# Kernel tuning notes

Measured on AMD Instinct MI355X. Metric: run time of the kernel, lower is better.

Reference implementation:

```python
import jax, jax.numpy as jnp
import numpy as np

EPS = 1e-08
CJS_WEIGHT = 0.5  # init kwarg `weight`
B, C = 4096, 8192


def setup_inputs() -> dict:
    key = jax.random.key(0)
    k1, k2 = jax.random.split(key)
    pred_logit = jax.random.normal(k1, (B, C), dtype=jnp.float32)
    gt_raw = jax.random.uniform(k2, (B, C), dtype=jnp.float32) + EPS
    gt = gt_raw / jnp.sum(gt_raw, axis=1, keepdims=True)  # row-stochastic target distribution
    return {"pred_logit": pred_logit, "gt": gt}


def reference(pred_logit, gt):
    xlogy = jax.scipy.special.xlogy
    n, c = pred_logit.shape

    # CrossEntropyLoss with soft (probability) targets, mean over batch
    logp = jax.nn.log_softmax(pred_logit, axis=1)
    ce = -jnp.mean(jnp.sum(gt * logp, axis=1))

    # CJS loss: sum_{i=1..C} 0.5*(KL(D_{:i} || m_{:i}) + KL(P_{:i} || m_{:i})) / B
    # Column j contributes to every prefix i > j, i.e. with weight (C - j):
    # one fused weighted-sum pass instead of the O(C^2) prefix loop.
    p = jnp.exp(logp)                      # softmax(pred_logit)
    m = 0.5 * (gt + p + EPS)
    logm = jnp.log(m)
    contrib = (xlogy(gt, gt) - gt * logm) + (xlogy(p, p) - p * logm)  # [B, C]
    w = (c - jnp.arange(c)).astype(pred_logit.dtype)                   # prefix multiplicity
    cjs = 0.5 * jnp.sum(contrib * w) / n   # 'batchmean' divides by B

    return ce + CJS_WEIGHT * cjs
```

## Files before the change

### kernel.cpp

```cpp
#include <hip/hip_runtime.h>

#define EPSF 1e-8f
#define NROWS 4096
#define NCOLS 8192
#define TPB 256
#define F4_PER_LANE (NCOLS / 4 / 64)

__global__ __launch_bounds__(TPB) void cecjs_main(const float* __restrict__ pred,
                                                  const float* __restrict__ gt,
                                                  double2* __restrict__ partial) {
    const int lane = threadIdx.x & 63;
    const int row  = blockIdx.x * (TPB / 64) + (threadIdx.x >> 6);

    const float4* pr = (const float4*)(pred + (size_t)row * NCOLS);
    const float4* gr = (const float4*)(gt   + (size_t)row * NCOLS);

    float s = 0.f;
    #pragma unroll 4
    for (int i = 0; i < F4_PER_LANE; ++i) {
        float4 v = pr[lane + i * 64];
        s += (__expf(v.x) + __expf(v.y)) + (__expf(v.z) + __expf(v.w));
    }
    #pragma unroll
    for (int off = 1; off < 64; off <<= 1) s += __shfl_xor(s, off, 64);
    const float logsum = __logf(s);

    float ce = 0.f, cj = 0.f;
    #pragma unroll 4
    for (int i = 0; i < F4_PER_LANE; ++i) {
        float4 v  = pr[lane + i * 64];
        float4 g4 = gr[lane + i * 64];
        const int c0 = (lane + i * 64) * 4;
        #pragma unroll
        for (int k = 0; k < 4; ++k) {
            float x  = (&v.x)[k];
            float g  = (&g4.x)[k];
            float lp = x - logsum;
            float p  = __expf(lp);
            ce = fmaf(g, lp, ce);
            float m    = 0.5f * (g + p + EPSF);
            float logm = __logf(m);
            float contrib = g * (__logf(g) - logm) + p * (lp - logm);
            cj = fmaf(contrib, (float)(NCOLS - (c0 + k)), cj);
        }
    }
    #pragma unroll
    for (int off = 1; off < 64; off <<= 1) {
        ce += __shfl_xor(ce, off, 64);
        cj += __shfl_xor(cj, off, 64);
    }
    if (lane == 0) partial[row] = make_double2((double)ce, (double)cj);
}

__global__ __launch_bounds__(1024) void cecjs_final(const double2* __restrict__ partial,
                                                    float* __restrict__ out) {
    __shared__ double sce[16], scj[16];
    const int tid  = threadIdx.x;
    const int lane = tid & 63;
    const int wid  = tid >> 6;
    double ce = 0.0, cj = 0.0;
    #pragma unroll
    for (int i = tid; i < NROWS; i += 1024) {
        double2 d = partial[i];
        ce += d.x; cj += d.y;
    }
    #pragma unroll
    for (int off = 1; off < 64; off <<= 1) {
        ce += __shfl_xor(ce, off, 64);
        cj += __shfl_xor(cj, off, 64);
    }
    if (lane == 0) { sce[wid] = ce; scj[wid] = cj; }
    __syncthreads();
    if (tid == 0) {
        double a = 0.0, b = 0.0;
        #pragma unroll
        for (int i = 0; i < 16; ++i) { a += sce[i]; b += scj[i]; }
        out[0] = (float)((-a + 0.25 * b) / (double)NROWS);
    }
}

extern "C" void kernel_launch(void* const* d_in, const int* in_sizes, int n_in,
                              void* d_out, int out_size, void* d_ws, size_t ws_size,
                              hipStream_t stream) {
    const float* pred = (const float*)d_in[0];
    const float* gt   = (const float*)d_in[1];
    double2* partial  = (double2*)d_ws;
    cecjs_main<<<NROWS / (TPB / 64), TPB, 0, stream>>>(pred, gt, partial);
    cecjs_final<<<1, 1024, 0, stream>>>(partial, (float*)d_out);
}
```

Before: 281.5 us.

## Map one row per block and keep pred values and exps in registers

Each row is now handled by a 512-thread block instead of a single wavefront, and each thread holds its 16 pred values in registers. The second global read of pred goes away and the exponentials are reused, so p becomes exp times a reciprocal of the row sum instead of a second exp. Cross-wave reductions now go through shared memory with two block barriers. Register pressure rises, and the barriers add some synchronisation cost per row.

```diff
diff --git a/kernel.cpp b/kernel.cpp
--- a/kernel.cpp
+++ b/kernel.cpp
@@ -3,45 +3,61 @@
 #define EPSF 1e-8f
 #define NROWS 4096
 #define NCOLS 8192
-#define TPB 256
-#define F4_PER_LANE (NCOLS / 4 / 64)
+#define TPB 512
 
 __global__ __launch_bounds__(TPB) void cecjs_main(const float* __restrict__ pred,
                                                   const float* __restrict__ gt,
                                                   double2* __restrict__ partial) {
-    const int lane = threadIdx.x & 63;
-    const int row  = blockIdx.x * (TPB / 64) + (threadIdx.x >> 6);
+    __shared__ float  sA[8];
+    __shared__ double sce[8], scj[8];
+
+    const int row  = blockIdx.x;
+    const int tid  = threadIdx.x;
+    const int lane = tid & 63;
+    const int wid  = tid >> 6;
 
     const float4* pr = (const float4*)(pred + (size_t)row * NCOLS);
     const float4* gr = (const float4*)(gt   + (size_t)row * NCOLS);
 
+    float4 v[4], e[4];
     float s = 0.f;
-    #pragma unroll 4
-    for (int i = 0; i < F4_PER_LANE; ++i) {
-        float4 v = pr[lane + i * 64];
-        s += (__expf(v.x) + __expf(v.y)) + (__expf(v.z) + __expf(v.w));
+    #pragma unroll
+    for (int i = 0; i < 4; ++i) v[i] = pr[tid + i * TPB];
+    #pragma unroll
+    for (int i = 0; i < 4; ++i) {
+        e[i].x = __expf(v[i].x);
+        e[i].y = __expf(v[i].y);
+        e[i].z = __expf(v[i].z);
+        e[i].w = __expf(v[i].w);
+        s += (e[i].x + e[i].y) + (e[i].z + e[i].w);
     }
     #pragma unroll
     for (int off = 1; off < 64; off <<= 1) s += __shfl_xor(s, off, 64);
-    const float logsum = __logf(s);
+    if (lane == 0) sA[wid] = s;
+    __syncthreads();
+    float tot = 0.f;
+    #pragma unroll
+    for (int i = 0; i < 8; ++i) tot += sA[i];
+    const float logsum = __logf(tot);
+    const float invsum = 1.0f / tot;
 
     float ce = 0.f, cj = 0.f;
-    #pragma unroll 4
-    for (int i = 0; i < F4_PER_LANE; ++i) {
-        float4 v  = pr[lane + i * 64];
-        float4 g4 = gr[lane + i * 64];
-        const int c0 = (lane + i * 64) * 4;
+    #pragma unroll
+    for (int i = 0; i < 4; ++i) {
+        float4 g4 = gr[tid + i * TPB];
+        const float w0 = (float)(NCOLS - (tid + i * TPB) * 4);
         #pragma unroll
         for (int k = 0; k < 4; ++k) {
-            float x  = (&v.x)[k];
+            float x  = (&v[i].x)[k];
+            float ev = (&e[i].x)[k];
             float g  = (&g4.x)[k];
             float lp = x - logsum;
-            float p  = __expf(lp);
+            float p  = ev * invsum;
             ce = fmaf(g, lp, ce);
             float m    = 0.5f * (g + p + EPSF);
             float logm = __logf(m);
             float contrib = g * (__logf(g) - logm) + p * (lp - logm);
-            cj = fmaf(contrib, (float)(NCOLS - (c0 + k)), cj);
+            cj = fmaf(contrib, w0 - (float)k, cj);
         }
     }
     #pragma unroll
@@ -49,7 +65,14 @@
         ce += __shfl_xor(ce, off, 64);
         cj += __shfl_xor(cj, off, 64);
     }
-    if (lane == 0) partial[row] = make_double2((double)ce, (double)cj);
+    if (lane == 0) { sce[wid] = (double)ce; scj[wid] = (double)cj; }
+    __syncthreads();
+    if (tid == 0) {
+        double a = 0.0, b = 0.0;
+        #pragma unroll
+        for (int i = 0; i < 8; ++i) { a += sce[i]; b += scj[i]; }
+        partial[row] = make_double2(a, b);
+    }
 }
 
 __global__ __launch_bounds__(1024) void cecjs_final(const double2* __restrict__ partial,
@@ -85,6 +108,6 @@
     const float* pred = (const float*)d_in[0];
     const float* gt   = (const float*)d_in[1];
     double2* partial  = (double2*)d_ws;
-    cecjs_main<<<NROWS / (TPB / 64), TPB, 0, stream>>>(pred, gt, partial);
+    cecjs_main<<<NROWS, TPB, 0, stream>>>(pred, gt, partial);
     cecjs_final<<<1, 1024, 0, stream>>>(partial, (float*)d_out);
 }
```

New measurement: 277.5 us. About the same (-1.4%).

## Split row logsumexp into separate kernel and grid-stride the main elementwise pass

Applied to the files above, without the earlier changes.

Moves the per-row sum of exponentials into its own kernel, with one block per row, that writes log2 of the sum to workspace. The main kernel then walks the flattened arrays with a grid-stride loop over 2048 blocks, computing in base 2 with the native exp2/log2 intrinsics. It scales by ln2 once in the final reduction. This removes the one-wave-per-row serialization and mixes rows across blocks, at the cost of an extra launch and reading pred twice from global memory rather than from cache.

```diff
diff --git a/kernel.cpp b/kernel.cpp
--- a/kernel.cpp
+++ b/kernel.cpp
@@ -1,66 +1,98 @@
 #include <hip/hip_runtime.h>
 
-#define EPSF 1e-8f
-#define NROWS 4096
-#define NCOLS 8192
-#define TPB 256
-#define F4_PER_LANE (NCOLS / 4 / 64)
+#define EPSF   1e-8f
+#define NROWS  4096
+#define NCOLS  8192
+#define F4ROW  (NCOLS / 4)
+#define K2_BLOCKS 2048
+#define K2_TPB    256
+#define NTHREADS  (K2_BLOCKS * K2_TPB)
+#define ITERS     ((NROWS * F4ROW) / NTHREADS)
+#define LOG2E  1.44269504088896340736f
+#define LN2    0.693147180559945309417f
 
-__global__ __launch_bounds__(TPB) void cecjs_main(const float* __restrict__ pred,
-                                                  const float* __restrict__ gt,
-                                                  double2* __restrict__ partial) {
-    const int lane = threadIdx.x & 63;
-    const int row  = blockIdx.x * (TPB / 64) + (threadIdx.x >> 6);
+#if __has_builtin(__builtin_amdgcn_exp2f)
+#define EXP2F(x) __builtin_amdgcn_exp2f(x)
+#else
+#define EXP2F(x) exp2f(x)
+#endif
+#if __has_builtin(__builtin_amdgcn_logf)
+#define LOG2F(x) __builtin_amdgcn_logf(x)
+#else
+#define LOG2F(x) log2f(x)
+#endif
 
+__global__ __launch_bounds__(256) void k_rowsum(const float* __restrict__ pred,
+                                                float* __restrict__ ls2) {
+    __shared__ float sA[4];
+    const int row = blockIdx.x, tid = threadIdx.x, lane = tid & 63, wid = tid >> 6;
     const float4* pr = (const float4*)(pred + (size_t)row * NCOLS);
-    const float4* gr = (const float4*)(gt   + (size_t)row * NCOLS);
-
     float s = 0.f;
-    #pragma unroll 4
-    for (int i = 0; i < F4_PER_LANE; ++i) {
-        float4 v = pr[lane + i * 64];
-        s += (__expf(v.x) + __expf(v.y)) + (__expf(v.z) + __expf(v.w));
+    #pragma unroll
+    for (int i = 0; i < 8; ++i) {
+        float4 v = pr[tid + i * 256];
+        s += (EXP2F(v.x * LOG2E) + EXP2F(v.y * LOG2E))
+           + (EXP2F(v.z * LOG2E) + EXP2F(v.w * LOG2E));
     }
     #pragma unroll
     for (int off = 1; off < 64; off <<= 1) s += __shfl_xor(s, off, 64);
-    const float logsum = __logf(s);
+    if (lane == 0) sA[wid] = s;
+    __syncthreads();
+    if (tid == 0) ls2[row] = LOG2F(sA[0] + sA[1] + sA[2] + sA[3]);
+}
 
-    float ce = 0.f, cj = 0.f;
+__global__ __launch_bounds__(K2_TPB) void k_main(const float* __restrict__ pred,
+                                                 const float* __restrict__ gt,
+                                                 const float* __restrict__ ls2,
+                                                 double2* __restrict__ partial) {
+    __shared__ float sce[4], scj[4];
+    const int tid0 = blockIdx.x * K2_TPB + threadIdx.x;
+    const float4* pr = (const float4*)pred;
+    const float4* gr = (const float4*)gt;
+
+    float ce2 = 0.f, cj2 = 0.f;
     #pragma unroll 4
-    for (int i = 0; i < F4_PER_LANE; ++i) {
-        float4 v  = pr[lane + i * 64];
-        float4 g4 = gr[lane + i * 64];
-        const int c0 = (lane + i * 64) * 4;
+    for (int it = 0; it < ITERS; ++it) {
+        const int f  = tid0 + it * NTHREADS;
+        float4 v  = pr[f];
+        float4 g4 = gr[f];
+        float ls  = ls2[f >> 11];
+        const float wbase = (float)(NCOLS - ((f & (F4ROW - 1)) << 2));
         #pragma unroll
         for (int k = 0; k < 4; ++k) {
-            float x  = (&v.x)[k];
-            float g  = (&g4.x)[k];
-            float lp = x - logsum;
-            float p  = __expf(lp);
-            ce = fmaf(g, lp, ce);
-            float m    = 0.5f * (g + p + EPSF);
-            float logm = __logf(m);
-            float contrib = g * (__logf(g) - logm) + p * (lp - logm);
-            cj = fmaf(contrib, (float)(NCOLS - (c0 + k)), cj);
+            float x = (&v.x)[k], g = (&g4.x)[k];
+            float lp2 = fmaf(x, LOG2E, -ls);
+            float p   = EXP2F(lp2);
+            ce2 = fmaf(g, lp2, ce2);
+            float m   = fmaf(0.5f, g + p, 0.5f * EPSF);
+            float l2m = LOG2F(m);
+            float l2g = LOG2F(g);
+            float contrib = g * (l2g - l2m) + p * (lp2 - l2m);
+            cj2 = fmaf(contrib, wbase - (float)k, cj2);
         }
     }
+    const int lane = threadIdx.x & 63, wid = threadIdx.x >> 6;
     #pragma unroll
     for (int off = 1; off < 64; off <<= 1) {
-        ce += __shfl_xor(ce, off, 64);
-        cj += __shfl_xor(cj, off, 64);
+        ce2 += __shfl_xor(ce2, off, 64);
+        cj2 += __shfl_xor(cj2, off, 64);
     }
-    if (lane == 0) partial[row] = make_double2((double)ce, (double)cj);
+    if (lane == 0) { sce[wid] = ce2; scj[wid] = cj2; }
+    __syncthreads();
+    if (threadIdx.x == 0) {
+        double a = (double)sce[0] + (double)sce[1] + (double)sce[2] + (double)sce[3];
+        double b = (double)scj[0] + (double)scj[1] + (double)scj[2] + (double)scj[3];
+        partial[blockIdx.x] = make_double2(a, b);
+    }
 }
 
-__global__ __launch_bounds__(1024) void cecjs_final(const double2* __restrict__ partial,
-                                                    float* __restrict__ out) {
+__global__ __launch_bounds__(1024) void k_final(const double2* __restrict__ partial,
+                                                float* __restrict__ out) {
     __shared__ double sce[16], scj[16];
-    const int tid  = threadIdx.x;
-    const int lane = tid & 63;
-    const int wid  = tid >> 6;
+    const int tid = threadIdx.x, lane = tid & 63, wid = tid >> 6;
     double ce = 0.0, cj = 0.0;
     #pragma unroll
-    for (int i = tid; i < NROWS; i += 1024) {
+    for (int i = tid; i < K2_BLOCKS; i += 1024) {
         double2 d = partial[i];
         ce += d.x; cj += d.y;
     }
@@ -75,7 +107,7 @@
         double a = 0.0, b = 0.0;
         #pragma unroll
         for (int i = 0; i < 16; ++i) { a += sce[i]; b += scj[i]; }
-        out[0] = (float)((-a + 0.25 * b) / (double)NROWS);
+        out[0] = (float)(((-a + 0.25 * b) * (double)LN2) / (double)NROWS);
     }
 }
 
@@ -84,7 +116,9 @@
                               hipStream_t stream) {
     const float* pred = (const float*)d_in[0];
     const float* gt   = (const float*)d_in[1];
-    double2* partial  = (double2*)d_ws;
-    cecjs_main<<<NROWS / (TPB / 64), TPB, 0, stream>>>(pred, gt, partial);
-    cecjs_final<<<1, 1024, 0, stream>>>(partial, (float*)d_out);
+    float*   ls2     = (float*)d_ws;
+    double2* partial = (double2*)((char*)d_ws + NROWS * sizeof(float));
+    k_rowsum<<<NROWS, 256, 0, stream>>>(pred, ls2);
+    k_main<<<K2_BLOCKS, K2_TPB, 0, stream>>>(pred, gt, ls2, partial);
+    k_final<<<1, 1024, 0, stream>>>(partial, (float*)d_out);
 }
```

New measurement: 278.0 us. Within noise of the previous version (-1.2%).
